# Kernel tuning notes

Measured on AMD Instinct MI355X. Metric: run time of the kernel, lower is better.

Reference implementation:

```python
import jax, jax.numpy as jnp
import numpy as np

N_NODES = 100000
N_EDGES = 1000000
D_IN = 64
D_HID = 64


def gcn_conv(x, w, b, row, col, n_nodes):
    """PyG GCNConv: out = D^-1/2 (A + I) D^-1/2 (X W) + b."""
    xw = x @ w  # [N, H]
    sl = jnp.arange(n_nodes)
    r = jnp.concatenate([row, sl])  # add self-loops
    c = jnp.concatenate([col, sl])
    deg = jax.ops.segment_sum(jnp.ones(r.shape[0], dtype=xw.dtype), c,
                              num_segments=n_nodes)
    dinv = jnp.where(deg > 0, jax.lax.rsqrt(deg), 0.0)
    norm = dinv[r] * dinv[c]  # [E+N]
    msg = xw[r] * norm[:, None]  # gather + normalize
    out = jax.ops.segment_sum(msg, c, num_segments=n_nodes)  # scatter-add
    return out + b


def setup_inputs() -> dict:
    key = jax.random.key(0)
    k = jax.random.split(key, 8)
    x = jax.random.normal(k[0], (N_NODES, D_IN), dtype=jnp.float32)
    edge_index = jax.random.randint(k[1], (2, N_EDGES), 0, N_NODES, dtype=jnp.int64)
    s1 = 1.0 / np.sqrt(D_IN)
    s2 = 1.0 / np.sqrt(D_HID)
    w1 = jax.random.uniform(k[2], (D_IN, D_HID), jnp.float32, -s1, s1)
    b1 = jnp.zeros((D_HID,), jnp.float32)
    w2 = jax.random.uniform(k[3], (D_HID, D_HID), jnp.float32, -s2, s2)
    b2 = jnp.zeros((D_HID,), jnp.float32)
    sl = 1.0 / np.sqrt(2 * D_HID)
    w_lin = jax.random.uniform(k[4], (2 * D_HID, 1), jnp.float32, -sl, sl)
    b_lin = jax.random.uniform(k[5], (1,), jnp.float32, -sl, sl)
    return {"x": x, "edge_index": edge_index, "w1": w1, "b1": b1,
            "w2": w2, "b2": b2, "w_lin": w_lin, "b_lin": b_lin}


def reference(x, edge_index, w1, b1, w2, b2, w_lin, b_lin):
    row, col = edge_index[0], edge_index[1]
    n = x.shape[0]
    h = jax.nn.relu(gcn_conv(x, w1, b1, row, col, n))
    # dropout(0.5) is identity in eval mode
    h = jax.nn.relu(gcn_conv(h, w2, b2, row, col, n))
    edge_features = jnp.concatenate([h[row], h[col]], axis=1)  # [E, 2H]
    logits = edge_features @ w_lin + b_lin  # [E, 1]
    return jax.nn.sigmoid(logits).squeeze(-1)  # [E]
```

## Files before the change

kernel.cpp:

```cpp
#include <hip/hip_runtime.h>
#include <math.h>

#define D 64
#define SCAN_BLOCK 256
#define SCAN_ITEMS 4
#define SCAN_TILE (SCAN_BLOCK * SCAN_ITEMS)
#define NREG 8
#define FILL_CHUNK 4096

__device__ __forceinline__ unsigned short f2bf(float f) {
    union { float f; unsigned int i; } v; v.f = f;
    unsigned int u = v.i;
    unsigned int r = (u + 0x7FFFu + ((u >> 16) & 1u)) >> 16;
    return (unsigned short)r;
}
__device__ __forceinline__ float bf2f(unsigned short u) {
    union { unsigned int i; float f; } v; v.i = ((unsigned int)u) << 16;
    return v.f;
}

__global__ void zero_int_kernel(int* p, int n) {
    int i = blockIdx.x * blockDim.x + threadIdx.x;
    if (i < n) p[i] = 0;
}

__global__ void count_region_kernel(const int* __restrict__ col, int* cnt, int E, int n) {
    int r = blockIdx.x & (NREG - 1);
    int c = blockIdx.x >> 3;
    int lo = (int)(((long long)r * n) / NREG);
    int hi = (int)(((long long)(r + 1) * n) / NREG);
    int e0 = c * FILL_CHUNK;
    int e1 = min(E, e0 + FILL_CHUNK);
    for (int e = e0 + (int)threadIdx.x; e < e1; e += (int)blockDim.x) {
        int cl = col[e];
        if (cl >= lo && cl < hi) atomicAdd(&cnt[cl], 1);
    }
}

__global__ void block_reduce_kernel(const int* __restrict__ cnt, int* __restrict__ blockSums, int n) {
    int b = blockIdx.x, t = threadIdx.x;
    int base = b * SCAN_TILE + t * SCAN_ITEMS;
    int s = 0;
    #pragma unroll
    for (int k = 0; k < SCAN_ITEMS; ++k) {
        int i = base + k;
        if (i < n) s += cnt[i];
    }
    #pragma unroll
    for (int o = 32; o > 0; o >>= 1) s += __shfl_xor(s, o, 64);
    __shared__ int wsum[SCAN_BLOCK / 64];
    if ((t & 63) == 0) wsum[t >> 6] = s;
    __syncthreads();
    if (t == 0) {
        int tot = 0;
        #pragma unroll
        for (int w = 0; w < SCAN_BLOCK / 64; ++w) tot += wsum[w];
        blockSums[b] = tot;
    }
}

__global__ void scan_sums_kernel(int* blockSums, int nb) {
    __shared__ int sh[256];
    int t = threadIdx.x;
    int v = (t < nb) ? blockSums[t] : 0;
    sh[t] = v;
    __syncthreads();
    for (int o = 1; o < 256; o <<= 1) {
        int u = (t >= o) ? sh[t - o] : 0;
        __syncthreads();
        sh[t] += u;
        __syncthreads();
    }
    if (t < nb) blockSums[t] = (t == 0) ? 0 : sh[t - 1];
}

__global__ void scan_apply_kernel(const int* __restrict__ cnt, const int* __restrict__ blockSums,
                                  int* __restrict__ off, float* __restrict__ dinv, int n) {
    int b = blockIdx.x, t = threadIdx.x;
    int base = b * SCAN_TILE + t * SCAN_ITEMS;
    int c[SCAN_ITEMS];
    int s = 0;
    #pragma unroll
    for (int k = 0; k < SCAN_ITEMS; ++k) {
        int i = base + k;
        c[k] = (i < n) ? cnt[i] : 0;
        s += c[k];
    }
    __shared__ int sh[SCAN_BLOCK];
    sh[t] = s;
    __syncthreads();
    for (int o = 1; o < SCAN_BLOCK; o <<= 1) {
        int u = (t >= o) ? sh[t - o] : 0;
        __syncthreads();
        sh[t] += u;
        __syncthreads();
    }
    int run = blockSums[b] + ((t == 0) ? 0 : sh[t - 1]);
    #pragma unroll
    for (int k = 0; k < SCAN_ITEMS; ++k) {
        int i = base + k;
        if (i < n) {
            off[i] = run;
            run += c[k];
            dinv[i] = rsqrtf(1.0f + (float)c[k]);
        }
    }
}

__global__ void region_bounds_kernel(const int* __restrict__ off, int* __restrict__ colBound,
                                     int n, int E) {
    int k = threadIdx.x;
    if (k > NREG) return;
    if (k == 0) { colBound[0] = 0; return; }
    if (k == NREG) { colBound[NREG] = n; return; }
    long long target = ((long long)k * E) / NREG;
    int lo = 0, hi = n;
    while (lo < hi) {
        int mid = (lo + hi) >> 1;
        if ((long long)off[mid] < target) lo = mid + 1; else hi = mid;
    }
    colBound[k] = lo;
}

__global__ void fill_region_kernel(const int* __restrict__ row, const int* __restrict__ col,
                                   const int* __restrict__ colBound,
                                   int* off, int* __restrict__ adj, int E) {
    int r = blockIdx.x & (NREG - 1);
    int c = blockIdx.x >> 3;
    int lo = colBound[r], hi = colBound[r + 1];
    int e0 = c * FILL_CHUNK;
    int e1 = min(E, e0 + FILL_CHUNK);
    for (int e = e0 + (int)threadIdx.x; e < e1; e += (int)blockDim.x) {
        int cl = col[e];
        if (cl >= lo && cl < hi) {
            int pos = atomicAdd(&off[cl], 1);
            adj[pos] = row[e];
        }
    }
}

__device__ __forceinline__ float4 fma4(float s, float4 w, float4 a) {
    a.x = fmaf(s, w.x, a.x); a.y = fmaf(s, w.y, a.y);
    a.z = fmaf(s, w.z, a.z); a.w = fmaf(s, w.w, a.w);
    return a;
}

__global__ void gemm64_reg_kernel(const float* __restrict__ X, const float* __restrict__ W,
                                  unsigned short* __restrict__ Y, int n, int applyRelu) {
    int gtid = blockIdx.x * blockDim.x + threadIdx.x;
    int wv = gtid >> 6;
    int nw = (gridDim.x * blockDim.x) >> 6;
    int lane = threadIdx.x & 63;
    int c4 = lane & 15;
    int kg = lane >> 4;

    float4 wreg[16];
    #pragma unroll
    for (int t = 0; t < 16; ++t)
        wreg[t] = ((const float4*)W)[(kg * 16 + t) * 16 + c4];

    for (int r = wv; r < n; r += nw) {
        const float4* xr = (const float4*)(X + (size_t)r * D) + kg * 4;
        float4 acc = make_float4(0.f, 0.f, 0.f, 0.f);
        #pragma unroll
        for (int t4 = 0; t4 < 4; ++t4) {
            float4 xv = xr[t4];
            if (applyRelu) {
                xv.x = fmaxf(xv.x, 0.f); xv.y = fmaxf(xv.y, 0.f);
                xv.z = fmaxf(xv.z, 0.f); xv.w = fmaxf(xv.w, 0.f);
            }
            acc = fma4(xv.x, wreg[t4 * 4 + 0], acc);
            acc = fma4(xv.y, wreg[t4 * 4 + 1], acc);
            acc = fma4(xv.z, wreg[t4 * 4 + 2], acc);
            acc = fma4(xv.w, wreg[t4 * 4 + 3], acc);
        }
        acc.x += __shfl_xor(acc.x, 16, 64); acc.y += __shfl_xor(acc.y, 16, 64);
        acc.z += __shfl_xor(acc.z, 16, 64); acc.w += __shfl_xor(acc.w, 16, 64);
        acc.x += __shfl_xor(acc.x, 32, 64); acc.y += __shfl_xor(acc.y, 32, 64);
        acc.z += __shfl_xor(acc.z, 32, 64); acc.w += __shfl_xor(acc.w, 32, 64);
        if (lane < 16) {
            ushort4 o;
            o.x = f2bf(acc.x); o.y = f2bf(acc.y);
            o.z = f2bf(acc.z); o.w = f2bf(acc.w);
            ((ushort4*)(Y + (size_t)r * D))[c4] = o;
        }
    }
}

template <int DOTS>
__global__ void agg_kernel(const unsigned short* __restrict__ xw, const float* __restrict__ dinv,
                           const int* __restrict__ off, const int* __restrict__ adj,
                           const float* __restrict__ b, float* __restrict__ out,
                           const float* __restrict__ wlin,
                           float* __restrict__ adot, float* __restrict__ bdot, int n) {
    int wid = blockIdx.x * 4 + (threadIdx.x >> 6);
    if (wid >= n) return;
    int lane = threadIdx.x & 63;
    int l = lane & 15;
    int g = lane >> 4;
    int start = (wid == 0) ? 0 : off[wid - 1];
    int end = off[wid];
    int deg = end - start;
    float di = dinv[wid];
    const ushort4* xwb = (const ushort4*)xw;

    float4 acc = make_float4(0.f, 0.f, 0.f, 0.f);
    if (g == 0) {
        ushort4 u = xwb[(size_t)wid * 16 + l];
        float4 bb = ((const float4*)b)[l];
        float s = di * di;
        acc.x = fmaf(bf2f(u.x), s, bb.x); acc.y = fmaf(bf2f(u.y), s, bb.y);
        acc.z = fmaf(bf2f(u.z), s, bb.z); acc.w = fmaf(bf2f(u.w), s, bb.w);
    }

    for (int base = 0; base < deg; base += 64) {
        int k = base + lane;
        int a = 0; float s = 0.f;
        if (k < deg) {
            a = adj[start + k];
            s = dinv[a] * di;
        }
        int m = min(64, deg - base);
        int mm = (m + 7) & ~7;
        for (int kk = g; kk < mm; kk += 8) {
            int r0 = __shfl(a, kk, 64);
            int r1 = __shfl(a, kk + 4, 64);
            float s0 = __shfl(s, kk, 64);
            float s1 = __shfl(s, kk + 4, 64);
            ushort4 u0 = xwb[(size_t)r0 * 16 + l];
            ushort4 u1 = xwb[(size_t)r1 * 16 + l];
            acc.x = fmaf(bf2f(u0.x), s0, acc.x); acc.y = fmaf(bf2f(u0.y), s0, acc.y);
            acc.z = fmaf(bf2f(u0.z), s0, acc.z); acc.w = fmaf(bf2f(u0.w), s0, acc.w);
            acc.x = fmaf(bf2f(u1.x), s1, acc.x); acc.y = fmaf(bf2f(u1.y), s1, acc.y);
            acc.z = fmaf(bf2f(u1.z), s1, acc.z); acc.w = fmaf(bf2f(u1.w), s1, acc.w);
        }
    }
    acc.x += __shfl_xor(acc.x, 16, 64); acc.y += __shfl_xor(acc.y, 16, 64);
    acc.z += __shfl_xor(acc.z, 16, 64); acc.w += __shfl_xor(acc.w, 16, 64);
    acc.x += __shfl_xor(acc.x, 32, 64); acc.y += __shfl_xor(acc.y, 32, 64);
    acc.z += __shfl_xor(acc.z, 32, 64); acc.w += __shfl_xor(acc.w, 32, 64);

    if (DOTS) {
        float4 hv = acc;
        hv.x = fmaxf(hv.x, 0.f); hv.y = fmaxf(hv.y, 0.f);
        hv.z = fmaxf(hv.z, 0.f); hv.w = fmaxf(hv.w, 0.f);
        float4 wa = ((const float4*)wlin)[l];
        float4 wb = ((const float4*)wlin)[16 + l];
        float pa = hv.x * wa.x + hv.y * wa.y + hv.z * wa.z + hv.w * wa.w;
        float pb = hv.x * wb.x + hv.y * wb.y + hv.z * wb.z + hv.w * wb.w;
        #pragma unroll
        for (int o = 8; o > 0; o >>= 1) {
            pa += __shfl_xor(pa, o, 64);
            pb += __shfl_xor(pb, o, 64);
        }
        if (lane == 0) { adot[wid] = pa; bdot[wid] = pb; }
    } else {
        if (lane < 16)
            ((float4*)(out + (size_t)wid * D))[l] = acc;
    }
}

__global__ void edge_out_kernel(const int* __restrict__ row, const int* __restrict__ col,
                                const float* __restrict__ adot, const float* __restrict__ bdot,
                                const float* __restrict__ blin, float* __restrict__ out, int E) {
    int e = blockIdx.x * blockDim.x + threadIdx.x;
    if (e >= E) return;
    float z = adot[row[e]] + bdot[col[e]] + blin[0];
    out[e] = 1.f / (1.f + expf(-z));
}

extern "C" void kernel_launch(void* const* d_in, const int* in_sizes, int n_in,
                              void* d_out, int out_size, void* d_ws, size_t ws_size,
                              hipStream_t stream) {
    const float* x     = (const float*)d_in[0];
    const int*   ei    = (const int*)d_in[1];
    const float* w1    = (const float*)d_in[2];
    const float* b1    = (const float*)d_in[3];
    const float* w2    = (const float*)d_in[4];
    const float* b2    = (const float*)d_in[5];
    const float* w_lin = (const float*)d_in[6];
    const float* b_lin = (const float*)d_in[7];
    float* out = (float*)d_out;

    int n = in_sizes[0] / D;
    int E = in_sizes[1] / 2;
    const int* row = ei;
    const int* col = ei + E;

    char* ws = (char*)d_ws;
    size_t cur = 0;
    auto alloc = [&](size_t bytes) -> void* {
        void* p = ws + cur;
        cur += (bytes + 255) / 256 * 256;
        return p;
    };
    int nScanBlocks = (n + SCAN_TILE - 1) / SCAN_TILE;
    int*            cnt    = (int*)   alloc((size_t)n * sizeof(int));
    int*            off    = (int*)   alloc((size_t)n * sizeof(int));
    float*          dinv   = (float*) alloc((size_t)n * sizeof(float));
    int*            bsums  = (int*)   alloc((size_t)nScanBlocks * sizeof(int));
    int*            cbound = (int*)   alloc((size_t)(NREG + 1) * sizeof(int));
    int*            adj    = (int*)   alloc((size_t)E * sizeof(int));
    float*          adot   = (float*) alloc((size_t)n * sizeof(float));
    float*          bdot   = (float*) alloc((size_t)n * sizeof(float));
    unsigned short* bufA   = (unsigned short*)alloc((size_t)n * D * sizeof(unsigned short));
    float*          bufB   = (float*) alloc((size_t)n * D * sizeof(float));

    const int BT = 256;
    int gN     = (n + BT - 1) / BT;
    int gE     = (E + BT - 1) / BT;
    int gWave  = (n + 3) / 4;
    int gGemm  = 1024;
    int nChunk = (E + FILL_CHUNK - 1) / FILL_CHUNK;
    int gReg   = nChunk * NREG;

    zero_int_kernel<<<gN, BT, 0, stream>>>(cnt, n);
    count_region_kernel<<<gReg, BT, 0, stream>>>(col, cnt, E, n);
    block_reduce_kernel<<<nScanBlocks, SCAN_BLOCK, 0, stream>>>(cnt, bsums, n);
    scan_sums_kernel<<<1, 256, 0, stream>>>(bsums, nScanBlocks);
    scan_apply_kernel<<<nScanBlocks, SCAN_BLOCK, 0, stream>>>(cnt, bsums, off, dinv, n);
    region_bounds_kernel<<<1, 64, 0, stream>>>(off, cbound, n, E);
    fill_region_kernel<<<gReg, BT, 0, stream>>>(row, col, cbound, off, adj, E);

    gemm64_reg_kernel<<<gGemm, BT, 0, stream>>>(x, w1, bufA, n, 0);
    agg_kernel<0><<<gWave, BT, 0, stream>>>(bufA, dinv, off, adj, b1, bufB,
                                            nullptr, nullptr, nullptr, n);

    gemm64_reg_kernel<<<gGemm, BT, 0, stream>>>(bufB, w2, bufA, n, 1);
    agg_kernel<1><<<gWave, BT, 0, stream>>>(bufA, dinv, off, adj, b2, nullptr,
                                            w_lin, adot, bdot, n);

    edge_out_kernel<<<gE, BT, 0, stream>>>(row, col, adot, bdot, b_lin, out, E);
}
```

Baseline: 337.9 us.

## Build CSR via two-level bucket sort with shared-memory atomics

```diff
diff --git a/kernel.cpp b/kernel.cpp
--- a/kernel.cpp
+++ b/kernel.cpp
@@ -5,8 +5,7 @@
 #define SCAN_BLOCK 256
 #define SCAN_ITEMS 4
 #define SCAN_TILE (SCAN_BLOCK * SCAN_ITEMS)
-#define NREG 8
-#define FILL_CHUNK 4096
+#define NB_SHIFT 9
 
 __device__ __forceinline__ unsigned short f2bf(float f) {
     union { float f; unsigned int i; } v; v.f = f;
@@ -19,22 +18,19 @@
     return v.f;
 }
 
-__global__ void zero_int_kernel(int* p, int n) {
-    int i = blockIdx.x * blockDim.x + threadIdx.x;
-    if (i < n) p[i] = 0;
-}
-
-__global__ void count_region_kernel(const int* __restrict__ col, int* cnt, int E, int n) {
-    int r = blockIdx.x & (NREG - 1);
-    int c = blockIdx.x >> 3;
-    int lo = (int)(((long long)r * n) / NREG);
-    int hi = (int)(((long long)(r + 1) * n) / NREG);
-    int e0 = c * FILL_CHUNK;
-    int e1 = min(E, e0 + FILL_CHUNK);
-    for (int e = e0 + (int)threadIdx.x; e < e1; e += (int)blockDim.x) {
-        int cl = col[e];
-        if (cl >= lo && cl < hi) atomicAdd(&cnt[cl], 1);
-    }
+__global__ void hist_kernel(const int* __restrict__ col, int* __restrict__ histG,
+                            int E, int B, int NB, int CH) {
+    __shared__ int h[512];
+    int b = blockIdx.x, t = threadIdx.x;
+    for (int i = t; i < NB; i += blockDim.x) h[i] = 0;
+    __syncthreads();
+    int e0 = b * CH, e1 = min(E, e0 + CH);
+    for (int e = e0 + t; e < e1; e += blockDim.x) {
+        int c = __builtin_nontemporal_load(col + e);
+        atomicAdd(&h[c >> NB_SHIFT], 1);
+    }
+    __syncthreads();
+    for (int i = t; i < NB; i += blockDim.x) histG[i * B + b] = h[i];
 }
 
 __global__ void block_reduce_kernel(const int* __restrict__ cnt, int* __restrict__ blockSums, int n) {
@@ -75,7 +71,7 @@
 }
 
 __global__ void scan_apply_kernel(const int* __restrict__ cnt, const int* __restrict__ blockSums,
-                                  int* __restrict__ off, float* __restrict__ dinv, int n) {
+                                  int* __restrict__ outArr, float* __restrict__ dinv, int n) {
     int b = blockIdx.x, t = threadIdx.x;
     int base = b * SCAN_TILE + t * SCAN_ITEMS;
     int c[SCAN_ITEMS];
@@ -100,42 +96,64 @@
     for (int k = 0; k < SCAN_ITEMS; ++k) {
         int i = base + k;
         if (i < n) {
-            off[i] = run;
+            outArr[i] = run;
             run += c[k];
-            dinv[i] = rsqrtf(1.0f + (float)c[k]);
-        }
-    }
-}
-
-__global__ void region_bounds_kernel(const int* __restrict__ off, int* __restrict__ colBound,
-                                     int n, int E) {
-    int k = threadIdx.x;
-    if (k > NREG) return;
-    if (k == 0) { colBound[0] = 0; return; }
-    if (k == NREG) { colBound[NREG] = n; return; }
-    long long target = ((long long)k * E) / NREG;
-    int lo = 0, hi = n;
-    while (lo < hi) {
-        int mid = (lo + hi) >> 1;
-        if ((long long)off[mid] < target) lo = mid + 1; else hi = mid;
-    }
-    colBound[k] = lo;
-}
-
-__global__ void fill_region_kernel(const int* __restrict__ row, const int* __restrict__ col,
-                                   const int* __restrict__ colBound,
-                                   int* off, int* __restrict__ adj, int E) {
-    int r = blockIdx.x & (NREG - 1);
-    int c = blockIdx.x >> 3;
-    int lo = colBound[r], hi = colBound[r + 1];
-    int e0 = c * FILL_CHUNK;
-    int e1 = min(E, e0 + FILL_CHUNK);
-    for (int e = e0 + (int)threadIdx.x; e < e1; e += (int)blockDim.x) {
-        int cl = col[e];
-        if (cl >= lo && cl < hi) {
-            int pos = atomicAdd(&off[cl], 1);
-            adj[pos] = row[e];
-        }
+            if (dinv) dinv[i] = rsqrtf(1.0f + (float)c[k]);
+        }
+    }
+}
+
+__global__ void scatter_pairs_kernel(const int* __restrict__ row, const int* __restrict__ col,
+                                     const int* __restrict__ scanH, int2* __restrict__ pairs,
+                                     int E, int B, int NB, int CH) {
+    __shared__ int cur[512];
+    int b = blockIdx.x, t = threadIdx.x;
+    for (int i = t; i < NB; i += blockDim.x) cur[i] = scanH[i * B + b];
+    __syncthreads();
+    int e0 = b * CH, e1 = min(E, e0 + CH);
+    for (int e = e0 + t; e < e1; e += blockDim.x) {
+        int c = __builtin_nontemporal_load(col + e);
+        int r = __builtin_nontemporal_load(row + e);
+        int pos = atomicAdd(&cur[c >> NB_SHIFT], 1);
+        pairs[pos] = make_int2(r, c);
+    }
+}
+
+__global__ void bucket_csr_kernel(const int2* __restrict__ pairs, const int* __restrict__ scanH,
+                                  int* __restrict__ off, float* __restrict__ dinv,
+                                  int* __restrict__ adj, int E, int B, int NB, int n) {
+    __shared__ int cnt[512];
+    __shared__ int curs[512];
+    __shared__ int psum[256];
+    int k = blockIdx.x, t = threadIdx.x;
+    int nodeBase = k << NB_SHIFT;
+    int eStart = scanH[k * B];
+    int eEnd = (k == NB - 1) ? E : scanH[(k + 1) * B];
+    cnt[t] = 0; cnt[t + 256] = 0;
+    __syncthreads();
+    for (int e = eStart + t; e < eEnd; e += 256)
+        atomicAdd(&cnt[pairs[e].y - nodeBase], 1);
+    __syncthreads();
+    int c0 = cnt[2 * t], c1 = cnt[2 * t + 1];
+    psum[t] = c0 + c1;
+    __syncthreads();
+    for (int o = 1; o < 256; o <<= 1) {
+        int u = (t >= o) ? psum[t - o] : 0;
+        __syncthreads();
+        psum[t] += u;
+        __syncthreads();
+    }
+    int base = (t == 0) ? 0 : psum[t - 1];
+    int node0 = nodeBase + 2 * t, node1 = node0 + 1;
+    if (node0 < n) { off[node0] = eStart + base + c0;      dinv[node0] = rsqrtf(1.0f + (float)c0); }
+    if (node1 < n) { off[node1] = eStart + base + c0 + c1; dinv[node1] = rsqrtf(1.0f + (float)c1); }
+    curs[2 * t]     = eStart + base;
+    curs[2 * t + 1] = eStart + base + c0;
+    __syncthreads();
+    for (int e = eStart + t; e < eEnd; e += 256) {
+        int2 p = pairs[e];
+        int pos = atomicAdd(&curs[p.y - nodeBase], 1);
+        adj[pos] = p.x;
     }
 }
 
@@ -287,6 +305,12 @@
     const int* row = ei;
     const int* col = ei + E;
 
+    int NB = (n + (1 << NB_SHIFT) - 1) >> NB_SHIFT;
+    int B  = NB;
+    int CH = (E + B - 1) / B;
+    int NBB = NB * B;
+    int nScanBlocks = (NBB + SCAN_TILE - 1) / SCAN_TILE;
+
     char* ws = (char*)d_ws;
     size_t cur = 0;
     auto alloc = [&](size_t bytes) -> void* {
@@ -294,33 +318,29 @@
         cur += (bytes + 255) / 256 * 256;
         return p;
     };
-    int nScanBlocks = (n + SCAN_TILE - 1) / SCAN_TILE;
-    int*            cnt    = (int*)   alloc((size_t)n * sizeof(int));
-    int*            off    = (int*)   alloc((size_t)n * sizeof(int));
-    float*          dinv   = (float*) alloc((size_t)n * sizeof(float));
-    int*            bsums  = (int*)   alloc((size_t)nScanBlocks * sizeof(int));
-    int*            cbound = (int*)   alloc((size_t)(NREG + 1) * sizeof(int));
-    int*            adj    = (int*)   alloc((size_t)E * sizeof(int));
-    float*          adot   = (float*) alloc((size_t)n * sizeof(float));
-    float*          bdot   = (float*) alloc((size_t)n * sizeof(float));
-    unsigned short* bufA   = (unsigned short*)alloc((size_t)n * D * sizeof(unsigned short));
-    float*          bufB   = (float*) alloc((size_t)n * D * sizeof(float));
+    int*            histG = (int*)   alloc((size_t)NBB * sizeof(int));
+    int*            scanH = (int*)   alloc((size_t)NBB * sizeof(int));
+    int*            bsums = (int*)   alloc((size_t)nScanBlocks * sizeof(int));
+    int2*           pairs = (int2*)  alloc((size_t)E * sizeof(int2));
+    int*            off   = (int*)   alloc((size_t)n * sizeof(int));
+    float*          dinv  = (float*) alloc((size_t)n * sizeof(float));
+    int*            adj   = (int*)   alloc((size_t)E * sizeof(int));
+    float*          adot  = (float*) alloc((size_t)n * sizeof(float));
+    float*          bdot  = (float*) alloc((size_t)n * sizeof(float));
+    unsigned short* bufA  = (unsigned short*)alloc((size_t)n * D * sizeof(unsigned short));
+    float*          bufB  = (float*) alloc((size_t)n * D * sizeof(float));
 
     const int BT = 256;
-    int gN     = (n + BT - 1) / BT;
-    int gE     = (E + BT - 1) / BT;
-    int gWave  = (n + 3) / 4;
-    int gGemm  = 1024;
-    int nChunk = (E + FILL_CHUNK - 1) / FILL_CHUNK;
-    int gReg   = nChunk * NREG;
-
-    zero_int_kernel<<<gN, BT, 0, stream>>>(cnt, n);
-    count_region_kernel<<<gReg, BT, 0, stream>>>(col, cnt, E, n);
-    block_reduce_kernel<<<nScanBlocks, SCAN_BLOCK, 0, stream>>>(cnt, bsums, n);
+    int gE    = (E + BT - 1) / BT;
+    int gWave = (n + 3) / 4;
+    int gGemm = 1024;
+
+    hist_kernel<<<B, BT, 0, stream>>>(col, histG, E, B, NB, CH);
+    block_reduce_kernel<<<nScanBlocks, SCAN_BLOCK, 0, stream>>>(histG, bsums, NBB);
     scan_sums_kernel<<<1, 256, 0, stream>>>(bsums, nScanBlocks);
-    scan_apply_kernel<<<nScanBlocks, SCAN_BLOCK, 0, stream>>>(cnt, bsums, off, dinv, n);
-    region_bounds_kernel<<<1, 64, 0, stream>>>(off, cbound, n, E);
-    fill_region_kernel<<<gReg, BT, 0, stream>>>(row, col, cbound, off, adj, E);
+    scan_apply_kernel<<<nScanBlocks, SCAN_BLOCK, 0, stream>>>(histG, bsums, scanH, nullptr, NBB);
+    scatter_pairs_kernel<<<B, BT, 0, stream>>>(row, col, scanH, pairs, E, B, NB, CH);
+    bucket_csr_kernel<<<NB, BT, 0, stream>>>(pairs, scanH, off, dinv, adj, E, B, NB, n);
 
     gemm64_reg_kernel<<<gGemm, BT, 0, stream>>>(x, w1, bufA, n, 0);
     agg_kernel<0><<<gWave, BT, 0, stream>>>(bufA, dinv, off, adj, b1, bufB,
```

Result: faster. 276.0 us (-18.3%).
